# Optimization experiments

Measured on AMD Instinct MI355X. Metric: run time of the kernel, lower is better.

## Reference

```python
import jax, jax.numpy as jnp
import numpy as np
from jax import lax

KS = 3           # kernel size
PAD = 1          # padding
BN_EPS = 1e-5


def _conv(x, w, b):
    # plain stride-1, pad-1 NCHW conv
    y = lax.conv_general_dilated(x, w, window_strides=(1, 1),
                                 padding=[(PAD, PAD), (PAD, PAD)],
                                 dimension_numbers=("NCHW", "OIHW", "NCHW"))
    return y + b[None, :, None, None]


def _deform_conv(x, offset, mask, w_reg):
    # x: [B,C,H,W]; offset: [B,2K,H,W] (dy,dx interleaved); mask: [B,K,H,W]
    B, C, H, W = x.shape
    K = KS * KS
    dy = offset[:, 0::2]  # [B,K,H,W]
    dx = offset[:, 1::2]
    base_ky = jnp.repeat(jnp.arange(KS), KS).astype(x.dtype)   # [K]
    base_kx = jnp.tile(jnp.arange(KS), KS).astype(x.dtype)
    gy = (jnp.arange(H) - PAD).astype(x.dtype)
    gx = (jnp.arange(W) - PAD).astype(x.dtype)
    py = base_ky[None, :, None, None] + gy[None, None, :, None] + dy  # [B,K,H,W]
    px = base_kx[None, :, None, None] + gx[None, None, None, :] + dx

    y0 = jnp.floor(py); x0 = jnp.floor(px)
    wy = py - y0;       wx = px - x0
    x_flat = x.reshape(B, C, H * W)

    def gather(yi, xi):
        valid = (yi >= 0) & (yi < H) & (xi >= 0) & (xi < W)
        yc = jnp.clip(yi, 0, H - 1).astype(jnp.int32)
        xc = jnp.clip(xi, 0, W - 1).astype(jnp.int32)
        idx = (yc * W + xc).reshape(B, 1, K * H * W)
        v = jnp.take_along_axis(x_flat, jnp.broadcast_to(idx, (B, C, K * H * W)), axis=2)
        v = v.reshape(B, C, K, H, W)
        return v * valid[:, None].astype(x.dtype)

    sampled = ((1 - wy) * (1 - wx))[:, None] * gather(y0, x0) \
            + ((1 - wy) * wx)[:, None]       * gather(y0, x0 + 1) \
            + (wy * (1 - wx))[:, None]       * gather(y0 + 1, x0) \
            + (wy * wx)[:, None]             * gather(y0 + 1, x0 + 1)
    sampled = sampled * mask[:, None]  # modulation, [B,C,K,H,W]
    Cout = w_reg.shape[0]
    return jnp.einsum("bckhw,ock->bohw", sampled, w_reg.reshape(Cout, C, K))


def setup_inputs() -> dict:
    key = jax.random.key(0)
    ks = jax.random.split(key, 9)
    B, Cin, Cout, H, W = 4, 256, 256, 64, 64
    K = KS * KS
    inp = {
        "x": jax.random.normal(ks[0], (B, Cin, H, W), jnp.float32),
        # offset / modulator conv params (zero-init in source; small random for meaningful test)
        "w_off": jax.random.normal(ks[1], (2 * K, Cin, KS, KS), jnp.float32) * 0.01,
        "b_off": jax.random.normal(ks[2], (2 * K,), jnp.float32) * 0.01,
        "w_mod": jax.random.normal(ks[3], (K, Cin, KS, KS), jnp.float32) * 0.01,
        "b_mod": jax.random.normal(ks[4], (K,), jnp.float32) * 0.01,
        # regular conv weight (bias=False)
        "w_reg": jax.random.normal(ks[5], (Cout, Cin, KS, KS), jnp.float32) * (1.0 / np.sqrt(Cin * K)),
        # BatchNorm (inference mode: running stats)
        "gamma": jnp.ones((Cout,), jnp.float32),
        "beta": jnp.zeros((Cout,), jnp.float32),
        "run_mean": jax.random.normal(ks[6], (Cout,), jnp.float32) * 0.1,
        "run_var": jax.random.uniform(ks[7], (Cout,), jnp.float32, 0.5, 1.5),
    }
    return inp


def reference(x, w_off, b_off, w_mod, b_mod, w_reg, gamma, beta, run_mean, run_var):
    offset = _conv(x, w_off, b_off)                       # [B,2K,H,W]
    mask = 2.0 * jax.nn.sigmoid(_conv(x, w_mod, b_mod))   # [B,K,H,W]
    y = _deform_conv(x, offset, mask, w_reg)              # [B,Cout,H,W]
    inv = gamma / jnp.sqrt(run_var + BN_EPS)
    y = y * inv[None, :, None, None] + (beta - run_mean * inv)[None, :, None, None]
    return jax.nn.relu(y)
```

## Files before the change

### kernel.cpp

```cpp
#include <hip/hip_runtime.h>
#include <hip/hip_bf16.h>

typedef unsigned short u16;
typedef unsigned int   u32;
typedef short   bf16x8 __attribute__((ext_vector_type(8)));
typedef float   f32x4  __attribute__((ext_vector_type(4)));

__device__ __forceinline__ float bf2f(u16 u) {
    u32 t = ((u32)u) << 16;
    return __builtin_bit_cast(float, t);
}
__device__ __forceinline__ u32 f2bf(float f) {
    u32 u = __builtin_bit_cast(u32, f);
    return (u + 0x7FFFu + ((u >> 16) & 1u)) >> 16;
}
__device__ __forceinline__ void load_lds16(const u16* g, u16* l) {
    __builtin_amdgcn_global_load_lds(
        (const __attribute__((address_space(1))) u32*)(const void*)g,
        (__attribute__((address_space(3))) u32*)(void*)l, 16, 0, 0);
}
__device__ __forceinline__ uint4 gload4(const u16* sbase, u32 voff) {
    uint4 r;
    asm volatile("global_load_dwordx4 %0, %1, %2"
                 : "=v"(r) : "v"(voff), "s"(sbase) : "memory");
    return r;
}
__device__ __forceinline__ f32x4 gload4f(const float* sbase, u32 voff) {
    f32x4 r;
    asm volatile("global_load_dwordx4 %0, %1, %2"
                 : "=v"(r) : "v"(voff), "s"(sbase) : "memory");
    return r;
}
#define WAITVM(N) do { asm volatile("s_waitcnt vmcnt(" #N ")" ::: "memory"); \
                       __builtin_amdgcn_sched_barrier(0); } while (0)


__global__ void kprep(const float* __restrict__ woff, const float* __restrict__ wmod,
                      u16* __restrict__ ah, u16* __restrict__ al) {
    int i = blockIdx.x * 256 + threadIdx.x;
    if (i >= 32 * 2304) return;
    int oc = i / 2304, r = i - oc * 2304;
    int t = r >> 8, c = r & 255;
    float v = 0.f;
    if (oc < 18)      v = woff[oc * 2304 + c * 9 + t];
    else if (oc < 27) v = wmod[(oc - 18) * 2304 + c * 9 + t];
    u32 hb = f2bf(v);
    u32 lb = f2bf(v - bf2f((u16)hb));
    ah[i] = (u16)hb;
    al[i] = (u16)lb;
}

__global__ void kwreg(const float* __restrict__ wreg, u16* __restrict__ wregb) {
    int i = blockIdx.x * 256 + threadIdx.x;
    int o = i / 2304, r = i - o * 2304;
    int t = r >> 8, c = r & 255;
    wregb[i] = (u16)f2bf(wreg[o * 2304 + c * 9 + t]);
}

__global__ __launch_bounds__(256) void ktrans(const float* __restrict__ x,
                                              float* __restrict__ xt) {
    __shared__ float T[64][65];
    int t = threadIdx.x;
    int pl = t & 63, cr = t >> 6;
    int p0 = blockIdx.x * 64;
    int c0 = blockIdx.y * 64;
    int b  = blockIdx.z;
    const float* xb  = x  + ((long)b << 20);
    float*       xtb = xt + ((long)b << 20);
#pragma unroll
    for (int i = 0; i < 16; i++) {
        int c = cr + i * 4;
        T[c][pl] = xb[((long)(c0 + c) << 12) + p0 + pl];
    }
    __syncthreads();
#pragma unroll
    for (int i = 0; i < 16; i++) {
        int p = cr + i * 4;
        xtb[(long)(p0 + p) * 256 + c0 + pl] = T[pl][p];
    }
}

__global__ __launch_bounds__(256) void koffg(const float* __restrict__ xt,
                                             const u16* __restrict__ ah_g,
                                             const u16* __restrict__ al_g,
                                             const float* __restrict__ boff,
                                             const float* __restrict__ bmod,
                                             float* __restrict__ offf) {
    __shared__ u16 Ah[2][32 * 72], Al[2][32 * 72];
    __shared__ u16 Bh[2][32 * 72], Bl[2][32 * 72];
    int tid = threadIdx.x;
    int bid = blockIdx.x;
    int xcd = bid & 7, j = bid >> 3;
    int img = xcd >> 1;
    int row = ((xcd & 1) << 5) + (j >> 1);
    int n0 = ((img << 6) + row) * 64 + (j & 1) * 32;
    int b = n0 >> 12, h0 = (n0 & 4095) >> 6, w0 = n0 & 63;
    int lane = tid & 63, wv = tid >> 6;
    int mt = wv & 1, nt = wv >> 1;
    int col = lane & 15, quad = lane >> 4;

    int aoc = tid >> 3, ak0 = (tid & 7) * 8;
    int nl = tid & 31, cl0 = (tid >> 5) * 8;

    const float* xtb = xt + ((long)b << 20);
    u32 avoff0 = (u32)(aoc * 2304 + ak0) * 2;

    f32x4 acc = (f32x4){0.f, 0.f, 0.f, 0.f};

    uint4 pah, pal;
    f32x4 xw0, xw1;
    bool  vm;

    auto issue = [&](int kt) {
        int t = kt >> 2, c0 = (kt & 3) << 6, r0 = kt * 64;
        int dy = t / 3 - 1, dx = t % 3 - 1;
        pah = gload4(ah_g, avoff0 + (u32)r0 * 2);
        pal = gload4(al_g, avoff0 + (u32)r0 * 2);
        int hp = h0 + dy, wp = w0 + nl + dx;
        vm = ((unsigned)hp < 64u) && ((unsigned)wp < 64u);
        int hc = min(max(hp, 0), 63), wc = min(max(wp, 0), 63);
        u32 pixb = (u32)(hc * 64 + wc) << 10;
        u32 cb   = (u32)(c0 + cl0) << 2;
        xw0 = gload4f(xtb, pixb + cb);
        xw1 = gload4f(xtb, pixb + cb + 16);
    };
    auto stores = [&](int buf) {
        u32 whi[4], wlo[4];
#pragma unroll
        for (int i = 0; i < 8; i++) {
            float xvi = (i < 4) ? xw0[i] : xw1[i - 4];
            float v = vm ? xvi : 0.f;
            u32 hb = f2bf(v);
            u32 lb = f2bf(v - bf2f((u16)hb));
            if (i & 1) { whi[i >> 1] |= hb << 16; wlo[i >> 1] |= lb << 16; }
            else       { whi[i >> 1]  = hb;       wlo[i >> 1]  = lb; }
        }
        *(uint4*)&Ah[buf][aoc * 72 + ak0] = pah;
        *(uint4*)&Al[buf][aoc * 72 + ak0] = pal;
        *(uint4*)&Bh[buf][nl * 72 + cl0] = make_uint4(whi[0], whi[1], whi[2], whi[3]);
        *(uint4*)&Bl[buf][nl * 72 + cl0] = make_uint4(wlo[0], wlo[1], wlo[2], wlo[3]);
    };

    issue(0);
    WAITVM(0);
    stores(0);
    issue(1);
    asm volatile("s_waitcnt lgkmcnt(0)" ::: "memory");
    __builtin_amdgcn_s_barrier();
    __builtin_amdgcn_sched_barrier(0);

    for (int kt = 0; kt < 36; kt++) {
        int cur = kt & 1, nxt = kt + 1;
#pragma unroll
        for (int ks = 0; ks < 2; ks++) {
            int ko = ks * 32 + quad * 8;
            bf16x8 fah = *(const bf16x8*)&Ah[cur][(mt * 16 + col) * 72 + ko];
            bf16x8 fal = *(const bf16x8*)&Al[cur][(mt * 16 + col) * 72 + ko];
            bf16x8 fbh = *(const bf16x8*)&Bh[cur][(nt * 16 + col) * 72 + ko];
            bf16x8 fbl = *(const bf16x8*)&Bl[cur][(nt * 16 + col) * 72 + ko];
            acc = __builtin_amdgcn_mfma_f32_16x16x32_bf16(fah, fbh, acc, 0, 0, 0);
            acc = __builtin_amdgcn_mfma_f32_16x16x32_bf16(fah, fbl, acc, 0, 0, 0);
            acc = __builtin_amdgcn_mfma_f32_16x16x32_bf16(fal, fbh, acc, 0, 0, 0);
        }
        if (nxt < 36) {
            WAITVM(0);
            stores(nxt & 1);
            if (nxt + 1 < 36) issue(nxt + 1);
        }
        asm volatile("s_waitcnt lgkmcnt(0)" ::: "memory");
        __builtin_amdgcn_s_barrier();
        __builtin_amdgcn_sched_barrier(0);
    }

    int n = n0 + nt * 16 + col;
#pragma unroll
    for (int r = 0; r < 4; r++) {
        int oc = mt * 16 + quad * 4 + r;
        float s = acc[r];
        if (oc < 18) {
            int ch = 3 * (oc >> 1) + (oc & 1);
            offf[(ch << 14) + n] = s + boff[oc];
        } else if (oc < 27) {
            float tt = s + bmod[oc - 18];
            int ch = 3 * (oc - 18) + 2;
            offf[(ch << 14) + n] = 2.f / (1.f + __expf(-tt));
        }
    }
}

__global__ __launch_bounds__(512, 2) void kfused(const float* __restrict__ xt,
                                                 const float* __restrict__ offf,
                                                 const u16* __restrict__ wregb,
                                                 const float* __restrict__ gamma,
                                                 const float* __restrict__ beta,
                                                 const float* __restrict__ rmean,
                                                 const float* __restrict__ rvar,
                                                 float* __restrict__ out) {
    __shared__ u16 Wl[2][256 * 64];
    __shared__ u16 Sl[2][8 * 64 * 8];
    int tid = threadIdx.x;
    int lane = tid & 63, wv = tid >> 6;
    int pxs = lane >> 4, chq = lane & 15;
    int bid = blockIdx.x;
    int xcd = bid & 7;
    int bb  = xcd >> 1;
    int h   = ((xcd & 1) << 5) + (bid >> 3);
    int nbase = ((bb << 6) + h) * 64;
    int wo = (wv >> 1) * 64, wn = (wv & 1) * 32;
    int col = lane & 15, quad = lane >> 4;

    int px0 = wv * 8 + pxs;
    int px1 = wv * 8 + 4 + pxs;

    const float* xb = xt + ((long)bb << 20);

    f32x4 acc[4][2];
#pragma unroll
    for (int i = 0; i < 4; i++)
#pragma unroll
        for (int j = 0; j < 2; j++) acc[i][j] = (f32x4){0.f, 0.f, 0.f, 0.f};

    u32   pb0[4], pb1[4];
    float sw0[4], sw1[4];
    f32x4 g0[4], g1[4];

    auto tapcomp = [&](int t, int pxi, u32 (&pb)[4], float (&sw)[4]) {
        int n = nbase + pxi;
        int g = t / 3, tx = t - 3 * g;
        float dy = offf[((3 * t + 0) << 14) + n];
        float dx = offf[((3 * t + 1) << 14) + n];
        float m  = offf[((3 * t + 2) << 14) + n];
        float py = (float)(h - 1 + g) + dy;
        float px = (float)(pxi - 1 + tx) + dx;
        float y0f = floorf(py), x0f = floorf(px);
        float wy = py - y0f, wx = px - x0f;
        int iy0 = (int)y0f, ix0 = (int)x0f;
        int iy1 = iy0 + 1, ix1 = ix0 + 1;
        bool vy0 = (unsigned)iy0 < 64u, vy1 = (unsigned)iy1 < 64u;
        bool vx0 = (unsigned)ix0 < 64u, vx1 = (unsigned)ix1 < 64u;
        int cy0 = min(max(iy0, 0), 63), cy1 = min(max(iy1, 0), 63);
        int cx0 = min(max(ix0, 0), 63), cx1 = min(max(ix1, 0), 63);
        pb[0] = (u32)(cy0 * 64 + cx0) << 10; pb[1] = (u32)(cy0 * 64 + cx1) << 10;
        pb[2] = (u32)(cy1 * 64 + cx0) << 10; pb[3] = (u32)(cy1 * 64 + cx1) << 10;
        float a = 1.f - wy, bw = 1.f - wx;
        sw[0] = (vy0 && vx0) ? a  * bw * m : 0.f;
        sw[1] = (vy0 && vx1) ? a  * wx * m : 0.f;
        sw[2] = (vy1 && vx0) ? wy * bw * m : 0.f;
        sw[3] = (vy1 && vx1) ? wy * wx * m : 0.f;
    };
    auto gissue = [&](int kt) {
        u32 co = ((u32)(kt & 3) << 8) + (u32)chq * 16;
#pragma unroll
        for (int nb = 0; nb < 4; nb++) g0[nb] = gload4f(xb, pb0[nb] + co);
#pragma unroll
        for (int nb = 0; nb < 4; nb++) g1[nb] = gload4f(xb, pb1[nb] + co);
    };
    auto dmaA = [&](int kt, int buf) {
#pragma unroll
        for (int i = 0; i < 4; i++) {
            int cidx = tid + i * 512;
            int o = cidx >> 3, qp = cidx & 7;
            int ql = qp ^ (o & 7);
            load_lds16(wregb + (long)o * 2304 + kt * 64 + ql * 8,
                       &Wl[buf][cidx * 8]);
        }
    };
    auto bwrite = [&](int buf) {
        f32x4 v = sw0[0] * g0[0] + sw0[1] * g0[1] + sw0[2] * g0[2] + sw0[3] * g0[3];
        u32 w0 = f2bf(v[0]) | (f2bf(v[1]) << 16);
        u32 w1 = f2bf(v[2]) | (f2bf(v[3]) << 16);
        *(uint2*)&Sl[buf][((chq >> 1) * 64 + px0) * 8 + (chq & 1) * 4] =
            make_uint2(w0, w1);
        v = sw1[0] * g1[0] + sw1[1] * g1[1] + sw1[2] * g1[2] + sw1[3] * g1[3];
        w0 = f2bf(v[0]) | (f2bf(v[1]) << 16);
        w1 = f2bf(v[2]) | (f2bf(v[3]) << 16);
        *(uint2*)&Sl[buf][((chq >> 1) * 64 + px1) * 8 + (chq & 1) * 4] =
            make_uint2(w0, w1);
    };

    tapcomp(0, px0, pb0, sw0);
    tapcomp(0, px1, pb1, sw1);
    gissue(0);
    dmaA(0, 0);
    WAITVM(0);
    bwrite(0);
    __syncthreads();

    for (int kt = 0; kt < 36; kt++) {
        int cur = kt & 1, nxt = kt + 1;
        if (nxt < 36) {
            if ((nxt & 3) == 0) {
                tapcomp(nxt >> 2, px0, pb0, sw0);
                tapcomp(nxt >> 2, px1, pb1, sw1);
            }
            gissue(nxt);
            dmaA(nxt, nxt & 1);
        }
#pragma unroll
        for (int ks = 0; ks < 2; ks++) {
            bf16x8 af[4], bfr[2];
#pragma unroll
            for (int i = 0; i < 4; i++) {
                int r = wo + i * 16 + col;
                int ph = (ks * 4 + quad) ^ (r & 7);
                af[i] = *(const bf16x8*)&Wl[cur][r * 64 + ph * 8];
            }
#pragma unroll
            for (int j = 0; j < 2; j++)
                bfr[j] = *(const bf16x8*)&Sl[cur][((ks * 4 + quad) * 64 +
                                                   (wn + j * 16 + col)) * 8];
#pragma unroll
            for (int i = 0; i < 4; i++)
#pragma unroll
                for (int j = 0; j < 2; j++)
                    acc[i][j] = __builtin_amdgcn_mfma_f32_16x16x32_bf16(
                        af[i], bfr[j], acc[i][j], 0, 0, 0);
        }
        if (nxt < 36) {
            WAITVM(4);
            bwrite(nxt & 1);
        }
        __syncthreads();
    }

#pragma unroll
    for (int i = 0; i < 4; i++) {
        int ob = wo + i * 16 + quad * 4;
        float inv[4], add[4];
#pragma unroll
        for (int r = 0; r < 4; r++) {
            int o = ob + r;
            float iv = gamma[o] * rsqrtf(rvar[o] + 1e-5f);
            inv[r] = iv; add[r] = beta[o] - rmean[o] * iv;
        }
#pragma unroll
        for (int j = 0; j < 2; j++) {
            int n_g = nbase + wn + j * 16 + col;
            int bq = n_g >> 12, hw = n_g & 4095;
            float* op = out + ((long)bq << 20) + hw;
#pragma unroll
            for (int r = 0; r < 4; r++) {
                float v = acc[i][j][r] * inv[r] + add[r];
                v = fmaxf(v, 0.f);
                op[(long)(ob + r) << 12] = v;
            }
        }
    }
}

extern "C" void kernel_launch(void* const* d_in, const int* in_sizes, int n_in,
                              void* d_out, int out_size, void* d_ws, size_t ws_size,
                              hipStream_t stream) {
    const float* x     = (const float*)d_in[0];
    const float* woff  = (const float*)d_in[1];
    const float* boff  = (const float*)d_in[2];
    const float* wmod  = (const float*)d_in[3];
    const float* bmod  = (const float*)d_in[4];
    const float* wreg  = (const float*)d_in[5];
    const float* gamma = (const float*)d_in[6];
    const float* beta  = (const float*)d_in[7];
    const float* rmean = (const float*)d_in[8];
    const float* rvar  = (const float*)d_in[9];
    float* out = (float*)d_out;

    char* ws = (char*)d_ws;
    u16*   wph   = (u16*)(ws);
    u16*   wpl   = (u16*)(ws + 0x40000u);
    float* offf  = (float*)(ws + 0x80000u);
    u16*   wregb = (u16*)(ws + 0x240000u);
    float* xt    = (float*)(ws + 0x400000u);

    kprep<<<288,  256, 0, stream>>>(woff, wmod, wph, wpl);
    kwreg<<<2304, 256, 0, stream>>>(wreg, wregb);
    ktrans<<<dim3(64, 4, 4), 256, 0, stream>>>(x, xt);
    koffg<<<512,  256, 0, stream>>>(xt, wph, wpl, boff, bmod, offf);
    kfused<<<256, 512, 0, stream>>>(xt, offf, wregb, gamma, beta,
                                    rmean, rvar, out);
}
```

Baseline: 185.5 us.

## Split fused deform-conv blocks into half-row tiles to double grid size

Each fused block now processes 32 output pixels instead of 64, doubling the grid to 512 blocks and giving each wave a 32x32 output tile with one sample per lane. This targets underutilization and latency hiding from having only one block per CU. In exchange every block reloads the full weight tile, doubling weight traffic, and the per-wave MFMA-to-LDS-load ratio drops.

Result: faster. 178.5 us (-3.8%).

```diff
diff --git a/kernel.cpp b/kernel.cpp
--- a/kernel.cpp
+++ b/kernel.cpp
@@ -188,7 +188,7 @@
     }
 }
 
-__global__ __launch_bounds__(512, 2) void kfused(const float* __restrict__ xt,
+__global__ __launch_bounds__(512, 4) void kfused(const float* __restrict__ xt,
                                                  const float* __restrict__ offf,
                                                  const u16* __restrict__ wregb,
                                                  const float* __restrict__ gamma,
@@ -197,41 +197,40 @@
                                                  const float* __restrict__ rvar,
                                                  float* __restrict__ out) {
     __shared__ u16 Wl[2][256 * 64];
-    __shared__ u16 Sl[2][8 * 64 * 8];
+    __shared__ u16 Sl[2][8 * 32 * 8];
     int tid = threadIdx.x;
     int lane = tid & 63, wv = tid >> 6;
-    int pxs = lane >> 4, chq = lane & 15;
+    int chq = lane & 15;
+    int plo = wv * 4 + (lane >> 4);
     int bid = blockIdx.x;
-    int xcd = bid & 7;
+    int xcd = bid & 7, jj = bid >> 3;
     int bb  = xcd >> 1;
-    int h   = ((xcd & 1) << 5) + (bid >> 3);
-    int nbase = ((bb << 6) + h) * 64;
-    int wo = (wv >> 1) * 64, wn = (wv & 1) * 32;
+    int h   = ((xcd & 1) << 5) + (jj >> 1);
+    int nbase = ((bb << 6) + h) * 64 + (jj & 1) * 32;
+    int wo = wv * 32;
     int col = lane & 15, quad = lane >> 4;
 
-    int px0 = wv * 8 + pxs;
-    int px1 = wv * 8 + 4 + pxs;
-
     const float* xb = xt + ((long)bb << 20);
 
-    f32x4 acc[4][2];
-#pragma unroll
-    for (int i = 0; i < 4; i++)
+    f32x4 acc[2][2];
+#pragma unroll
+    for (int i = 0; i < 2; i++)
 #pragma unroll
         for (int j = 0; j < 2; j++) acc[i][j] = (f32x4){0.f, 0.f, 0.f, 0.f};
 
-    u32   pb0[4], pb1[4];
-    float sw0[4], sw1[4];
-    f32x4 g0[4], g1[4];
-
-    auto tapcomp = [&](int t, int pxi, u32 (&pb)[4], float (&sw)[4]) {
-        int n = nbase + pxi;
-        int g = t / 3, tx = t - 3 * g;
+    u32   pb[4];
+    float sw[4];
+    f32x4 g[4];
+
+    auto tapcomp = [&](int t) {
+        int n = nbase + plo;
+        int w = n & 63;
+        int gy = t / 3, tx = t - 3 * gy;
         float dy = offf[((3 * t + 0) << 14) + n];
         float dx = offf[((3 * t + 1) << 14) + n];
         float m  = offf[((3 * t + 2) << 14) + n];
-        float py = (float)(h - 1 + g) + dy;
-        float px = (float)(pxi - 1 + tx) + dx;
+        float py = (float)(h - 1 + gy) + dy;
+        float px = (float)(w - 1 + tx) + dx;
         float y0f = floorf(py), x0f = floorf(px);
         float wy = py - y0f, wx = px - x0f;
         int iy0 = (int)y0f, ix0 = (int)x0f;
@@ -251,9 +250,7 @@
     auto gissue = [&](int kt) {
         u32 co = ((u32)(kt & 3) << 8) + (u32)chq * 16;
 #pragma unroll
-        for (int nb = 0; nb < 4; nb++) g0[nb] = gload4f(xb, pb0[nb] + co);
-#pragma unroll
-        for (int nb = 0; nb < 4; nb++) g1[nb] = gload4f(xb, pb1[nb] + co);
+        for (int nb = 0; nb < 4; nb++) g[nb] = gload4f(xb, pb[nb] + co);
     };
     auto dmaA = [&](int kt, int buf) {
 #pragma unroll
@@ -266,20 +263,14 @@
         }
     };
     auto bwrite = [&](int buf) {
-        f32x4 v = sw0[0] * g0[0] + sw0[1] * g0[1] + sw0[2] * g0[2] + sw0[3] * g0[3];
+        f32x4 v = sw[0] * g[0] + sw[1] * g[1] + sw[2] * g[2] + sw[3] * g[3];
         u32 w0 = f2bf(v[0]) | (f2bf(v[1]) << 16);
         u32 w1 = f2bf(v[2]) | (f2bf(v[3]) << 16);
-        *(uint2*)&Sl[buf][((chq >> 1) * 64 + px0) * 8 + (chq & 1) * 4] =
+        *(uint2*)&Sl[buf][((chq >> 1) * 32 + plo) * 8 + (chq & 1) * 4] =
             make_uint2(w0, w1);
-        v = sw1[0] * g1[0] + sw1[1] * g1[1] + sw1[2] * g1[2] + sw1[3] * g1[3];
-        w0 = f2bf(v[0]) | (f2bf(v[1]) << 16);
-        w1 = f2bf(v[2]) | (f2bf(v[3]) << 16);
-        *(uint2*)&Sl[buf][((chq >> 1) * 64 + px1) * 8 + (chq & 1) * 4] =
-            make_uint2(w0, w1);
-    };
-
-    tapcomp(0, px0, pb0, sw0);
-    tapcomp(0, px1, pb1, sw1);
+    };
+
+    tapcomp(0);
     gissue(0);
     dmaA(0, 0);
     WAITVM(0);
@@ -289,28 +280,25 @@
     for (int kt = 0; kt < 36; kt++) {
         int cur = kt & 1, nxt = kt + 1;
         if (nxt < 36) {
-            if ((nxt & 3) == 0) {
-                tapcomp(nxt >> 2, px0, pb0, sw0);
-                tapcomp(nxt >> 2, px1, pb1, sw1);
-            }
+            if ((nxt & 3) == 0) tapcomp(nxt >> 2);
             gissue(nxt);
             dmaA(nxt, nxt & 1);
         }
 #pragma unroll
         for (int ks = 0; ks < 2; ks++) {
-            bf16x8 af[4], bfr[2];
-#pragma unroll
-            for (int i = 0; i < 4; i++) {
+            bf16x8 af[2], bfr[2];
+#pragma unroll
+            for (int i = 0; i < 2; i++) {
                 int r = wo + i * 16 + col;
                 int ph = (ks * 4 + quad) ^ (r & 7);
                 af[i] = *(const bf16x8*)&Wl[cur][r * 64 + ph * 8];
             }
 #pragma unroll
             for (int j = 0; j < 2; j++)
-                bfr[j] = *(const bf16x8*)&Sl[cur][((ks * 4 + quad) * 64 +
-                                                   (wn + j * 16 + col)) * 8];
-#pragma unroll
-            for (int i = 0; i < 4; i++)
+                bfr[j] = *(const bf16x8*)&Sl[cur][((ks * 4 + quad) * 32 +
+                                                   (j * 16 + col)) * 8];
+#pragma unroll
+            for (int i = 0; i < 2; i++)
 #pragma unroll
                 for (int j = 0; j < 2; j++)
                     acc[i][j] = __builtin_amdgcn_mfma_f32_16x16x32_bf16(
@@ -324,7 +312,7 @@
     }
 
 #pragma unroll
-    for (int i = 0; i < 4; i++) {
+    for (int i = 0; i < 2; i++) {
         int ob = wo + i * 16 + quad * 4;
         float inv[4], add[4];
 #pragma unroll
@@ -335,7 +323,7 @@
         }
 #pragma unroll
         for (int j = 0; j < 2; j++) {
-            int n_g = nbase + wn + j * 16 + col;
+            int n_g = nbase + j * 16 + col;
             int bq = n_g >> 12, hw = n_g & 4095;
             float* op = out + ((long)bq << 20) + hw;
 #pragma unroll
@@ -374,6 +362,6 @@
     kwreg<<<2304, 256, 0, stream>>>(wreg, wregb);
     ktrans<<<dim3(64, 4, 4), 256, 0, stream>>>(x, xt);
     koffg<<<512,  256, 0, stream>>>(xt, wph, wpl, boff, bmod, offf);
-    kfused<<<256, 512, 0, stream>>>(xt, offf, wregb, gamma, beta,
+    kfused<<<512, 512, 0, stream>>>(xt, offf, wregb, gamma, beta,
                                     rmean, rvar, out);
 }
```
